# Kernel tuning notes

Measured on AMD Instinct MI355X. Metric: run time of the kernel, lower is better.

The kernel has to match this reference:

```python
import jax, jax.numpy as jnp
import numpy as np

STATE_DIM = 32
ACTION_DIM = 8
LATENT_DIM = 64
HIDDEN = 128
X_DIM = ACTION_DIM + 1  # t channel + actions
B = 4096
L = 128
N_SUB = 2  # fixed RK4 substeps per knot interval


def natural_cubic_coeffs(x):
    """Natural cubic spline on unit-spaced knots 0..L-1 (matches torchcde's
    implicit arange grid). x: [B, L, C]. Returns per-interval coeffs b, c, d
    ([B, L-1, C]) s.t. X(i+u) = x_i + b u + c u^2 + d u^3."""
    Bb, Ln, C = x.shape
    n = Ln - 2
    # tridiagonal system for interior second derivatives (natural BC: m0=mL-1=0)
    M = 4.0 * jnp.eye(n, dtype=x.dtype) + jnp.eye(n, k=1, dtype=x.dtype) + jnp.eye(n, k=-1, dtype=x.dtype)
    rhs = 6.0 * (x[:, 2:] - 2.0 * x[:, 1:-1] + x[:, :-2])  # [B, n, C]
    m_in = jnp.linalg.solve(M, rhs.transpose(1, 0, 2).reshape(n, -1))  # [n, B*C]
    m_in = m_in.reshape(n, Bb, C).transpose(1, 0, 2)
    zpad = jnp.zeros((Bb, 1, C), x.dtype)
    m = jnp.concatenate([zpad, m_in, zpad], axis=1)  # [B, L, C]
    b = (x[:, 1:] - x[:, :-1]) - (2.0 * m[:, :-1] + m[:, 1:]) / 6.0
    c = m[:, :-1] / 2.0
    d = (m[:, 1:] - m[:, :-1]) / 6.0
    return b, c, d


def setup_inputs() -> dict:
    key = jax.random.key(0)
    ks = jax.random.split(key, 8)
    s = jax.random.normal(ks[0], (B, L, STATE_DIM), dtype=jnp.float32)
    a = jax.random.normal(ks[1], (B, L, ACTION_DIM), dtype=jnp.float32)
    t = jnp.broadcast_to(jnp.arange(L, dtype=jnp.float32), (B, L)) + jnp.zeros((B, L), jnp.float32)

    def lin(k, fi, fo, scale=1.0):
        return (jax.random.normal(k, (fi, fo), dtype=jnp.float32) * (scale / np.sqrt(fi))).astype(jnp.float32)

    enc_W = lin(ks[2], STATE_DIM + ACTION_DIM + 1, LATENT_DIM)
    enc_b = jnp.zeros((LATENT_DIM,), jnp.float32)
    f_W1 = lin(ks[3], LATENT_DIM, HIDDEN, 0.5)
    f_b1 = jnp.zeros((HIDDEN,), jnp.float32)
    f_W2 = lin(ks[4], HIDDEN, LATENT_DIM * X_DIM, 0.1)  # small scale keeps the CDE stable over 127 time units
    f_b2 = jnp.zeros((LATENT_DIM * X_DIM,), jnp.float32)
    dec_W = lin(ks[5], LATENT_DIM, STATE_DIM)
    dec_b = jnp.zeros((STATE_DIM,), jnp.float32)
    return dict(s=s, a=a, t=t, enc_W=enc_W, enc_b=enc_b, f_W1=f_W1, f_b1=f_b1,
                f_W2=f_W2, f_b2=f_b2, dec_W=dec_W, dec_b=dec_b)


def reference(s, a, t, enc_W, enc_b, f_W1, f_b1, f_W2, f_b2, dec_W, dec_b):
    # control path X = [t, a] : [B, L, X_DIM]
    x = jnp.concatenate([t[..., None], a], axis=-1)
    cb, cc, cd = natural_cubic_coeffs(x)  # each [B, L-1, X_DIM]

    z0 = jnp.concatenate([s[:, 0], a[:, 0], t[:, 0:1]], axis=-1) @ enc_W + enc_b  # [B, latent]

    def vf(z):  # f(z): [B, latent] -> [B, latent, X_DIM]
        h = jax.nn.relu(z @ f_W1 + f_b1)
        return (h @ f_W2 + f_b2).reshape(-1, LATENT_DIM, X_DIM)

    hstep = 1.0 / N_SUB

    def interval(z, coef):
        bi, ci, di = coef  # [B, X_DIM] each, current interval spline coeffs

        def dzdu(z, u):
            dX = bi + 2.0 * ci * u + 3.0 * di * (u * u)  # dX/dt on this interval
            return jnp.einsum('blx,bx->bl', vf(z), dX)

        for k in range(N_SUB):  # small fixed unroll, not a data-dim loop
            u = k * hstep
            k1 = dzdu(z, u)
            k2 = dzdu(z + 0.5 * hstep * k1, u + 0.5 * hstep)
            k3 = dzdu(z + 0.5 * hstep * k2, u + 0.5 * hstep)
            k4 = dzdu(z + hstep * k3, u + hstep)
            z = z + (hstep / 6.0) * (k1 + 2.0 * k2 + 2.0 * k3 + k4)
        return z, z

    coefs = (cb.transpose(1, 0, 2), cc.transpose(1, 0, 2), cd.transpose(1, 0, 2))  # [L-1, B, X_DIM]
    _, zs = jax.lax.scan(interval, z0, coefs)  # zs: [L-1, B, latent]
    z = jnp.concatenate([z0[None], zs], axis=0).transpose(1, 0, 2)  # [B, L, latent]
    return z @ dec_W + dec_b  # [B, L, state_dim]
```

## Files before the change

### kernel.cpp

```cpp
#include <hip/hip_runtime.h>

#define Bsz 4096
#define Lsz 128
#define NI  127
#define SD  32
#define AD  8
#define LAT 64
#define HID 128
#define BT  16
#define THR 512

typedef float f32x2 __attribute__((ext_vector_type(2)));
typedef float f32x4 __attribute__((ext_vector_type(4)));

__global__ __launch_bounds__(256) void repack_w2(const float* __restrict__ W2,
                                                 float* __restrict__ W2p8,
                                                 float* __restrict__ W2c0){
  int idx = blockIdx.x*256 + threadIdx.x;
  if (idx < HID*LAT*8){
    int x = idx & 7; int jl = idx >> 3; int l = jl & 63; int j = jl >> 6;
    W2p8[idx] = W2[(j*LAT + l)*9 + x + 1];
  } else if (idx < HID*LAT*9){
    int jl = idx - HID*LAT*8;
    W2c0[jl] = W2[(size_t)jl*9];
  }
}

__global__ __launch_bounds__(256) void spline_kernel(const float* __restrict__ a,
                                                     float* __restrict__ m_ws){
  __shared__ float cp_s[126];
  if (threadIdx.x == 0){
    float c = 0.25f; cp_s[0] = c;
    for (int i=1;i<126;i++){ c = 1.0f/(4.0f - c); cp_s[i] = c; }
  }
  __syncthreads();
  int tid = blockIdx.x*256 + threadIdx.x;
  int b = tid >> 3, c8 = tid & 7;
  float dp[126];
  const float* ab = a + (size_t)b*Lsz*AD + c8;
  float x0 = ab[0];
  float x1 = ab[AD];
  for (int i=0;i<126;i++){
    float x2 = ab[(size_t)(i+2)*AD];
    float rhs = 6.0f*(x2 - 2.0f*x1 + x0);
    dp[i] = (i==0)? rhs*0.25f : (rhs - dp[i-1])*cp_s[i];
    x0 = x1; x1 = x2;
  }
  m_ws[tid] = 0.0f;
  m_ws[((size_t)127*Bsz)*8 + tid] = 0.0f;
  float mn = 0.0f;
  for (int k=125;k>=0;k--){
    mn = dp[k] - cp_s[k]*mn;
    m_ws[((size_t)(k+1)*Bsz)*8 + tid] = mn;
  }
}

#define DPP_XOR1(v) __int_as_float(__builtin_amdgcn_mov_dpp(__float_as_int(v), 0xB1, 0xF, 0xF, true))
#define DPP_XOR2(v) __int_as_float(__builtin_amdgcn_mov_dpp(__float_as_int(v), 0x4E, 0xF, 0xF, true))
#define SWZ_XOR4(v) __int_as_float(__builtin_amdgcn_ds_swizzle(__float_as_int(v), 0x101F))

#define PK_MUL_BCLO(d, w, x) asm("v_pk_mul_f32 %0, %1, %2 op_sel:[0,0] op_sel_hi:[0,1]" : "=v"(d) : "v"(w), "v"(x))
#define PK_MUL_BCHI(d, w, x) asm("v_pk_mul_f32 %0, %1, %2 op_sel:[1,0] op_sel_hi:[1,1]" : "=v"(d) : "v"(w), "v"(x))
#define PK_FMA_BCLO(acc, w, x) asm("v_pk_fma_f32 %0, %1, %2, %0 op_sel:[0,0,0] op_sel_hi:[0,1,1]" : "+v"(acc) : "v"(w), "v"(x))
#define PK_FMA_BCHI(acc, w, x) asm("v_pk_fma_f32 %0, %1, %2, %0 op_sel:[1,0,0] op_sel_hi:[1,1,1]" : "+v"(acc) : "v"(w), "v"(x))
#define PK_FMA(acc, a, b)      asm("v_pk_fma_f32 %0, %1, %2, %0" : "+v"(acc) : "v"(a), "v"(b))
#define PK_ADD(d, a, b)        asm("v_pk_add_f32 %0, %1, %2" : "=v"(d) : "v"(a), "v"(b))

#define LO2(v4) __builtin_shufflevector(v4, v4, 0, 1)
#define HI2(v4) __builtin_shufflevector(v4, v4, 2, 3)

__attribute__((amdgpu_waves_per_eu(2,2)))
__global__ __launch_bounds__(THR) void cde_integrate(
    const float* __restrict__ s, const float* __restrict__ a, const float* __restrict__ t,
    const float* __restrict__ encW, const float* __restrict__ encb,
    const float* __restrict__ W1, const float* __restrict__ b1,
    const float* __restrict__ b2, const float* __restrict__ decW, const float* __restrict__ decb,
    const float* __restrict__ W2p8, const float* __restrict__ W2c0, const float* __restrict__ m_ws,
    float* __restrict__ out)
{
  __shared__ float W1t[HID][LAT+4];
  __shared__ float hp[8][292];
  __shared__ float zp[8][132];
  __shared__ float dXp[5][8][20];
  __shared__ float dWs[LAT][SD];
  __shared__ float dbs[SD];

  const int tid = threadIdx.x;
  const int b0 = blockIdx.x * BT;
  const int ol = tid >> 3;
  const int jg = tid & 7;

  for (int i=tid;i<HID*LAT;i+=THR){ int j = i & (HID-1); int k = i >> 7; W1t[j][k] = W1[k*HID+j]; }
  for (int i=tid;i<LAT*SD;i+=THR)  ((float*)dWs)[i] = decW[i];
  if (tid < SD) dbs[tid] = decb[tid];

  f32x2 wpk[16][4]; f32x2 wc0pk[8];
  {
    #pragma unroll
    for (int jj=0;jj<16;jj++){
      const f32x2* p2 = (const f32x2*)&W2p8[((size_t)(jg*16+jj)*LAT + ol)*8];
      wpk[jj][0]=p2[0]; wpk[jj][1]=p2[1]; wpk[jj][2]=p2[2]; wpk[jj][3]=p2[3];
    }
    #pragma unroll
    for (int q=0;q<8;q++){
      wc0pk[q].x = W2c0[(jg*16+2*q)*LAT + ol];
      wc0pk[q].y = W2c0[(jg*16+2*q+1)*LAT + ol];
    }
    #pragma unroll
    for (int jj=0;jj<16;jj++){
      asm volatile("" : "+v"(wpk[jj][0]), "+v"(wpk[jj][1]), "+v"(wpk[jj][2]), "+v"(wpk[jj][3]));
    }
  }
  f32x2 b2p[4]; f32x2 b2c0v; f32x2 b1pair; f32x2 one11; one11.x = 1.f; one11.y = 1.f;
  {
    const float* bp = b2 + ol*9;
    b2c0v.x = bp[0]; b2c0v.y = 0.f;
    b2p[0].x = bp[1]; b2p[0].y = bp[2];
    b2p[1].x = bp[3]; b2p[1].y = bp[4];
    b2p[2].x = bp[5]; b2p[2].y = bp[6];
    b2p[3].x = bp[7]; b2p[3].y = bp[8];
    b1pair.x = b1[2*ol]; b1pair.y = b1[2*ol+1];
  }

  {
    const int bb8 = tid >> 6;
    const int li = tid & 63;
    #pragma unroll
    for (int h=0; h<2; h++){
      const int b = bb8 + 8*h;
      const float* sb = s + (size_t)(b0+b)*Lsz*SD;
      const float* ab = a + (size_t)(b0+b)*Lsz*AD;
      const float tv = t[(size_t)(b0+b)*Lsz];
      float acc = encb[li];
      #pragma unroll
      for (int k=0;k<SD;k++) acc = fmaf(sb[k], encW[k*LAT+li], acc);
      #pragma unroll
      for (int k=0;k<AD;k++) acc = fmaf(ab[k], encW[(SD+k)*LAT+li], acc);
      acc = fmaf(tv, encW[(SD+AD)*LAT+li], acc);
      zp[b>>1][li*2 + (b&1)] = acc;
    }
  }
  __syncthreads();

  {
    const int bb = tid >> 5; const int o = tid & 31; const int c = bb & 1;
    const float* zrow = &zp[bb>>1][0];
    float acc = dbs[o];
    #pragma unroll 16
    for (int k=0;k<LAT;k++) acc = fmaf(zrow[2*k+c], dWs[k][o], acc);
    out[((size_t)(b0+bb)*Lsz + 0)*SD + o] = acc;
  }

  float zb0, zb1, ka0 = 0.f, ka1 = 0.f;
  { f32x2 zr = *(const f32x2*)&zp[jg][2*ol]; zb0 = zr.x; zb1 = zr.y; }

  #pragma unroll 1
  for (int iv=0; iv<NI; iv++){
    for (int idx=tid; idx<5*BT*8; idx+=THR){
      int ui = idx >> 7; int r = idx & 127; int bb = r >> 3; int x8 = r & 7;
      float u = 0.25f*(float)ui;
      int gb = b0+bb;
      float m0 = m_ws[((size_t)iv    *Bsz + gb)*8 + x8];
      float m1 = m_ws[((size_t)(iv+1)*Bsz + gb)*8 + x8];
      float xd = a[((size_t)gb*Lsz + iv+1)*AD + x8] - a[((size_t)gb*Lsz + iv)*AD + x8];
      float cb = xd - (2.f*m0 + m1)*(1.f/6.f);
      float cc = 0.5f*m0;
      float cd = (m1 - m0)*(1.f/6.f);
      dXp[ui][bb>>1][x8*2 + (bb&1)] = cb + (2.f*cc)*u + (3.f*cd)*(u*u);
    }

    #pragma unroll 1
    for (int st=0; st<8; st++){
      const int ui = (st+1)>>1;
      const int mode = st & 3;
      __syncthreads();

      {
        const int j0 = 2*ol;
        f32x2 acc0, acc1;
        PK_MUL_BCLO(acc0, b1pair, one11);
        PK_MUL_BCHI(acc1, b1pair, one11);
        const f32x4* zrow = (const f32x4*)&zp[jg][0];
        const f32x4* w0r = (const f32x4*)&W1t[j0][0];
        const f32x4* w1r = (const f32x4*)&W1t[j0+1][0];
        #pragma unroll
        for (int k16=0;k16<16;k16++){
          f32x4 zqA = zrow[2*k16], zqB = zrow[2*k16+1];
          f32x4 w0q = w0r[k16], w1q = w1r[k16];
          f32x2 w0l = LO2(w0q), w0h = HI2(w0q), w1l = LO2(w1q), w1h = HI2(w1q);
          f32x2 zA0 = LO2(zqA), zA1 = HI2(zqA), zB0 = LO2(zqB), zB1 = HI2(zqB);
          PK_FMA_BCLO(acc0, w0l, zA0); PK_FMA_BCHI(acc0, w0l, zA1);
          PK_FMA_BCLO(acc0, w0h, zB0); PK_FMA_BCHI(acc0, w0h, zB1);
          PK_FMA_BCLO(acc1, w1l, zA0); PK_FMA_BCHI(acc1, w1l, zA1);
          PK_FMA_BCLO(acc1, w1h, zB0); PK_FMA_BCHI(acc1, w1h, zB1);
        }
        f32x4 hv;
        hv.x = fmaxf(acc0.x, 0.f); hv.y = fmaxf(acc0.y, 0.f);
        hv.z = fmaxf(acc1.x, 0.f); hv.w = fmaxf(acc1.y, 0.f);
        *(f32x4*)&hp[jg][(ol>>3)*36 + (ol&7)*4] = hv;
      }
      __syncthreads();

      f32x2 dz[8];
      #pragma unroll
      for (int p=0;p<8;p++){
        const f32x4* dxr = (const f32x4*)&dXp[ui][p][0];
        f32x4 d0=dxr[0], d1=dxr[1], d2=dxr[2], d3=dxr[3];
        f32x2 dx2[8] = {LO2(d0),HI2(d0),LO2(d1),HI2(d1),LO2(d2),HI2(d2),LO2(d3),HI2(d3)};
        const f32x4* hr = (const f32x4*)&hp[p][jg*36];
        f32x2 acc; acc.x = 0.f; acc.y = 0.f;
        #pragma unroll
        for (int jj2=0;jj2<8;jj2++){
          f32x4 hq = hr[jj2];
          f32x2 hl = LO2(hq), hh = HI2(hq);
          {
            f32x2 wd;
            PK_MUL_BCLO(wd, wpk[2*jj2][0], dx2[0]); PK_FMA_BCHI(wd, wpk[2*jj2][0], dx2[1]);
            PK_FMA_BCLO(wd, wpk[2*jj2][1], dx2[2]); PK_FMA_BCHI(wd, wpk[2*jj2][1], dx2[3]);
            PK_FMA_BCLO(wd, wpk[2*jj2][2], dx2[4]); PK_FMA_BCHI(wd, wpk[2*jj2][2], dx2[5]);
            PK_FMA_BCLO(wd, wpk[2*jj2][3], dx2[6]); PK_FMA_BCHI(wd, wpk[2*jj2][3], dx2[7]);
            PK_FMA_BCLO(wd, wc0pk[jj2], one11);
            PK_FMA(acc, hl, wd);
          }
          {
            f32x2 wd;
            PK_MUL_BCLO(wd, wpk[2*jj2+1][0], dx2[0]); PK_FMA_BCHI(wd, wpk[2*jj2+1][0], dx2[1]);
            PK_FMA_BCLO(wd, wpk[2*jj2+1][1], dx2[2]); PK_FMA_BCHI(wd, wpk[2*jj2+1][1], dx2[3]);
            PK_FMA_BCLO(wd, wpk[2*jj2+1][2], dx2[4]); PK_FMA_BCHI(wd, wpk[2*jj2+1][2], dx2[5]);
            PK_FMA_BCLO(wd, wpk[2*jj2+1][3], dx2[6]); PK_FMA_BCHI(wd, wpk[2*jj2+1][3], dx2[7]);
            PK_FMA_BCHI(wd, wc0pk[jj2], one11);
            PK_FMA(acc, hh, wd);
          }
        }
        dz[p] = acc;
      }

      const bool g1 = jg & 1;
      f32x2 n4[4];
      #pragma unroll
      for (int i=0;i<4;i++){
        f32x2 lo = dz[2*i], hi = dz[2*i+1];
        f32x2 send = g1 ? lo : hi;
        f32x2 recv; recv.x = DPP_XOR1(send.x); recv.y = DPP_XOR1(send.y);
        f32x2 keep = g1 ? hi : lo;
        PK_ADD(n4[i], keep, recv);
      }
      const bool g2 = jg & 2;
      f32x2 n2[2];
      #pragma unroll
      for (int i=0;i<2;i++){
        f32x2 lo = n4[2*i], hi = n4[2*i+1];
        f32x2 send = g2 ? lo : hi;
        f32x2 recv; recv.x = DPP_XOR2(send.x); recv.y = DPP_XOR2(send.y);
        f32x2 keep = g2 ? hi : lo;
        PK_ADD(n2[i], keep, recv);
      }
      const bool g4 = jg & 4;
      f32x2 res;
      {
        f32x2 lo = n2[0], hi = n2[1];
        f32x2 send = g4 ? lo : hi;
        f32x2 recv; recv.x = SWZ_XOR4(send.x); recv.y = SWZ_XOR4(send.y);
        f32x2 keep = g4 ? hi : lo;
        PK_ADD(res, keep, recv);
      }

      f32x2 bias2;
      {
        const f32x4* dxb = (const f32x4*)&dXp[ui][jg][0];
        f32x4 e0=dxb[0], e1=dxb[1], e2=dxb[2], e3=dxb[3];
        PK_MUL_BCLO(bias2, b2c0v, one11);
        PK_FMA_BCLO(bias2, b2p[0], LO2(e0)); PK_FMA_BCHI(bias2, b2p[0], HI2(e0));
        PK_FMA_BCLO(bias2, b2p[1], LO2(e1)); PK_FMA_BCHI(bias2, b2p[1], HI2(e1));
        PK_FMA_BCLO(bias2, b2p[2], LO2(e2)); PK_FMA_BCHI(bias2, b2p[2], HI2(e2));
        PK_FMA_BCLO(bias2, b2p[3], LO2(e3)); PK_FMA_BCHI(bias2, b2p[3], HI2(e3));
      }
      f32x2 dzm2; PK_ADD(dzm2, res, bias2);
      const float dz0 = dzm2.x, dz1 = dzm2.y;

      float zn0, zn1;
      if (mode == 0){
        ka0 = dz0; ka1 = dz1;
        zn0 = fmaf(0.25f, dz0, zb0); zn1 = fmaf(0.25f, dz1, zb1);
      } else if (mode == 1){
        ka0 = fmaf(2.f, dz0, ka0); ka1 = fmaf(2.f, dz1, ka1);
        zn0 = fmaf(0.25f, dz0, zb0); zn1 = fmaf(0.25f, dz1, zb1);
      } else if (mode == 2){
        ka0 = fmaf(2.f, dz0, ka0); ka1 = fmaf(2.f, dz1, ka1);
        zn0 = fmaf(0.5f, dz0, zb0); zn1 = fmaf(0.5f, dz1, zb1);
      } else {
        ka0 += dz0; ka1 += dz1;
        zb0 = fmaf(0.5f/6.f, ka0, zb0); zb1 = fmaf(0.5f/6.f, ka1, zb1);
        zn0 = zb0; zn1 = zb1;
      }
      f32x2 zw; zw.x = zn0; zw.y = zn1;
      *(f32x2*)&zp[jg][2*ol] = zw;
    }

    __syncthreads();
    {
      const int bb = tid >> 5; const int o = tid & 31; const int c = bb & 1;
      const float* zrow = &zp[bb>>1][0];
      float acc = dbs[o];
      #pragma unroll 16
      for (int k=0;k<LAT;k++) acc = fmaf(zrow[2*k+c], dWs[k][o], acc);
      out[((size_t)(b0+bb)*Lsz + (iv+1))*SD + o] = acc;
    }
  }
}

extern "C" void kernel_launch(void* const* d_in, const int* in_sizes, int n_in,
                              void* d_out, int out_size, void* d_ws, size_t ws_size,
                              hipStream_t stream){
  const float* s    = (const float*)d_in[0];
  const float* a    = (const float*)d_in[1];
  const float* t    = (const float*)d_in[2];
  const float* encW = (const float*)d_in[3];
  const float* encb = (const float*)d_in[4];
  const float* W1   = (const float*)d_in[5];
  const float* b1   = (const float*)d_in[6];
  const float* W2   = (const float*)d_in[7];
  const float* b2   = (const float*)d_in[8];
  const float* decW = (const float*)d_in[9];
  const float* decb = (const float*)d_in[10];
  float* out = (float*)d_out;
  float* ws  = (float*)d_ws;
  float* W2p8 = ws;
  float* W2c0 = ws + HID*LAT*8;
  float* m_ws = ws + HID*LAT*9;

  hipLaunchKernelGGL(repack_w2, dim3((HID*LAT*9+255)/256), dim3(256), 0, stream, W2, W2p8, W2c0);
  hipLaunchKernelGGL(spline_kernel, dim3(Bsz*8/256), dim3(256), 0, stream, a, m_ws);
  hipLaunchKernelGGL(cde_integrate, dim3(Bsz/BT), dim3(THR), 0, stream,
                     s,a,t,encW,encb,W1,b1,b2,decW,decb,W2p8,W2c0,m_ws,out);
}
```

Measured before the change: 8.486 ms.

## Double threads per block and split hidden/W2 reductions across lane pairs

Raises the block to 1024 threads with 4 waves per EU and splits the work of each output lane across 16 threads instead of 8. The first layer halves its K loop and combines the halves with a swizzle, and the second layer holds half as many W2 weights per thread in registers, adding one more xor-8 reduction step. The b2 bias is moved into shared memory. The aim is to cut per-thread register pressure and serial work so more waves hide latency, at the cost of extra cross-lane shuffles, and in the first layer half the threads do redundant work and sit idle at the write.

```diff
diff --git a/kernel.cpp b/kernel.cpp
--- a/kernel.cpp
+++ b/kernel.cpp
@@ -8,7 +8,7 @@
 #define LAT 64
 #define HID 128
 #define BT  16
-#define THR 512
+#define THR 1024
 
 typedef float f32x2 __attribute__((ext_vector_type(2)));
 typedef float f32x4 __attribute__((ext_vector_type(4)));
@@ -58,18 +58,18 @@
 #define DPP_XOR1(v) __int_as_float(__builtin_amdgcn_mov_dpp(__float_as_int(v), 0xB1, 0xF, 0xF, true))
 #define DPP_XOR2(v) __int_as_float(__builtin_amdgcn_mov_dpp(__float_as_int(v), 0x4E, 0xF, 0xF, true))
 #define SWZ_XOR4(v) __int_as_float(__builtin_amdgcn_ds_swizzle(__float_as_int(v), 0x101F))
+#define SWZ_XOR8(v) __int_as_float(__builtin_amdgcn_ds_swizzle(__float_as_int(v), 0x201F))
 
 #define PK_MUL_BCLO(d, w, x) asm("v_pk_mul_f32 %0, %1, %2 op_sel:[0,0] op_sel_hi:[0,1]" : "=v"(d) : "v"(w), "v"(x))
 #define PK_MUL_BCHI(d, w, x) asm("v_pk_mul_f32 %0, %1, %2 op_sel:[1,0] op_sel_hi:[1,1]" : "=v"(d) : "v"(w), "v"(x))
 #define PK_FMA_BCLO(acc, w, x) asm("v_pk_fma_f32 %0, %1, %2, %0 op_sel:[0,0,0] op_sel_hi:[0,1,1]" : "+v"(acc) : "v"(w), "v"(x))
 #define PK_FMA_BCHI(acc, w, x) asm("v_pk_fma_f32 %0, %1, %2, %0 op_sel:[1,0,0] op_sel_hi:[1,1,1]" : "+v"(acc) : "v"(w), "v"(x))
 #define PK_FMA(acc, a, b)      asm("v_pk_fma_f32 %0, %1, %2, %0" : "+v"(acc) : "v"(a), "v"(b))
-#define PK_ADD(d, a, b)        asm("v_pk_add_f32 %0, %1, %2" : "=v"(d) : "v"(a), "v"(b))
 
 #define LO2(v4) __builtin_shufflevector(v4, v4, 0, 1)
 #define HI2(v4) __builtin_shufflevector(v4, v4, 2, 3)
 
-__attribute__((amdgpu_waves_per_eu(2,2)))
+__attribute__((amdgpu_waves_per_eu(4,4)))
 __global__ __launch_bounds__(THR) void cde_integrate(
     const float* __restrict__ s, const float* __restrict__ a, const float* __restrict__ t,
     const float* __restrict__ encW, const float* __restrict__ encb,
@@ -79,70 +79,60 @@
     float* __restrict__ out)
 {
   __shared__ float W1t[HID][LAT+4];
-  __shared__ float hp[8][292];
+  __shared__ float hp[8][324];
   __shared__ float zp[8][132];
   __shared__ float dXp[5][8][20];
+  __shared__ float b2s[LAT][12];
   __shared__ float dWs[LAT][SD];
   __shared__ float dbs[SD];
 
   const int tid = threadIdx.x;
   const int b0 = blockIdx.x * BT;
-  const int ol = tid >> 3;
-  const int jg = tid & 7;
+  const int ol = tid >> 4;
+  const int jg = tid & 15;
+  const int pown = jg & 7;
+  const int kh = (tid >> 3) & 1;
+  const int bp = tid & 7;
 
   for (int i=tid;i<HID*LAT;i+=THR){ int j = i & (HID-1); int k = i >> 7; W1t[j][k] = W1[k*HID+j]; }
   for (int i=tid;i<LAT*SD;i+=THR)  ((float*)dWs)[i] = decW[i];
+  for (int i=tid;i<LAT*12;i+=THR){ int l=i/12, x=i%12; b2s[l][x] = (x<9)? b2[l*9+x] : 0.f; }
   if (tid < SD) dbs[tid] = decb[tid];
 
-  f32x2 wpk[16][4]; f32x2 wc0pk[8];
+  f32x2 wpk[8][4]; f32x2 wc0[4];
   {
     #pragma unroll
-    for (int jj=0;jj<16;jj++){
-      const f32x2* p2 = (const f32x2*)&W2p8[((size_t)(jg*16+jj)*LAT + ol)*8];
-      wpk[jj][0]=p2[0]; wpk[jj][1]=p2[1]; wpk[jj][2]=p2[2]; wpk[jj][3]=p2[3];
+    for (int jj=0;jj<8;jj++){
+      const f32x4* p4 = (const f32x4*)&W2p8[((size_t)(jg*8+jj)*LAT + ol)*8];
+      f32x4 A = p4[0], B = p4[1];
+      wpk[jj][0]=LO2(A); wpk[jj][1]=HI2(A); wpk[jj][2]=LO2(B); wpk[jj][3]=HI2(B);
     }
     #pragma unroll
-    for (int q=0;q<8;q++){
-      wc0pk[q].x = W2c0[(jg*16+2*q)*LAT + ol];
-      wc0pk[q].y = W2c0[(jg*16+2*q+1)*LAT + ol];
-    }
+    for (int q=0;q<4;q++){
+      wc0[q].x = W2c0[(jg*8+2*q)*LAT + ol];
+      wc0[q].y = W2c0[(jg*8+2*q+1)*LAT + ol];
+    }
+  }
+  f32x2 b1pair; b1pair.x = b1[2*ol]; b1pair.y = b1[2*ol+1];
+  f32x2 one11; one11.x = 1.f; one11.y = 1.f;
+
+  {
+    const int b = tid >> 6;
+    const int li = tid & 63;
+    const float* sb = s + (size_t)(b0+b)*Lsz*SD;
+    const float* ab = a + (size_t)(b0+b)*Lsz*AD;
+    const float tv = t[(size_t)(b0+b)*Lsz];
+    float acc = encb[li];
     #pragma unroll
-    for (int jj=0;jj<16;jj++){
-      asm volatile("" : "+v"(wpk[jj][0]), "+v"(wpk[jj][1]), "+v"(wpk[jj][2]), "+v"(wpk[jj][3]));
-    }
-  }
-  f32x2 b2p[4]; f32x2 b2c0v; f32x2 b1pair; f32x2 one11; one11.x = 1.f; one11.y = 1.f;
-  {
-    const float* bp = b2 + ol*9;
-    b2c0v.x = bp[0]; b2c0v.y = 0.f;
-    b2p[0].x = bp[1]; b2p[0].y = bp[2];
-    b2p[1].x = bp[3]; b2p[1].y = bp[4];
-    b2p[2].x = bp[5]; b2p[2].y = bp[6];
-    b2p[3].x = bp[7]; b2p[3].y = bp[8];
-    b1pair.x = b1[2*ol]; b1pair.y = b1[2*ol+1];
-  }
-
-  {
-    const int bb8 = tid >> 6;
-    const int li = tid & 63;
+    for (int k=0;k<SD;k++) acc = fmaf(sb[k], encW[k*LAT+li], acc);
     #pragma unroll
-    for (int h=0; h<2; h++){
-      const int b = bb8 + 8*h;
-      const float* sb = s + (size_t)(b0+b)*Lsz*SD;
-      const float* ab = a + (size_t)(b0+b)*Lsz*AD;
-      const float tv = t[(size_t)(b0+b)*Lsz];
-      float acc = encb[li];
-      #pragma unroll
-      for (int k=0;k<SD;k++) acc = fmaf(sb[k], encW[k*LAT+li], acc);
-      #pragma unroll
-      for (int k=0;k<AD;k++) acc = fmaf(ab[k], encW[(SD+k)*LAT+li], acc);
-      acc = fmaf(tv, encW[(SD+AD)*LAT+li], acc);
-      zp[b>>1][li*2 + (b&1)] = acc;
-    }
+    for (int k=0;k<AD;k++) acc = fmaf(ab[k], encW[(SD+k)*LAT+li], acc);
+    acc = fmaf(tv, encW[(SD+AD)*LAT+li], acc);
+    zp[b>>1][li*2 + (b&1)] = acc;
   }
   __syncthreads();
 
-  {
+  if (tid < BT*SD){
     const int bb = tid >> 5; const int o = tid & 31; const int c = bb & 1;
     const float* zrow = &zp[bb>>1][0];
     float acc = dbs[o];
@@ -151,13 +141,13 @@
     out[((size_t)(b0+bb)*Lsz + 0)*SD + o] = acc;
   }
 
-  float zb0, zb1, ka0 = 0.f, ka1 = 0.f;
-  { f32x2 zr = *(const f32x2*)&zp[jg][2*ol]; zb0 = zr.x; zb1 = zr.y; }
+  f32x2 zb, ka;
+  { zb = *(const f32x2*)&zp[pown][2*ol]; ka.x = 0.f; ka.y = 0.f; }
 
   #pragma unroll 1
   for (int iv=0; iv<NI; iv++){
-    for (int idx=tid; idx<5*BT*8; idx+=THR){
-      int ui = idx >> 7; int r = idx & 127; int bb = r >> 3; int x8 = r & 7;
+    if (tid < 5*BT*8){
+      int ui = tid >> 7; int r = tid & 127; int bb = r >> 3; int x8 = r & 7;
       float u = 0.25f*(float)ui;
       int gb = b0+bb;
       float m0 = m_ws[((size_t)iv    *Bsz + gb)*8 + x8];
@@ -176,129 +166,135 @@
       __syncthreads();
 
       {
-        const int j0 = 2*ol;
         f32x2 acc0, acc1;
         PK_MUL_BCLO(acc0, b1pair, one11);
         PK_MUL_BCHI(acc1, b1pair, one11);
-        const f32x4* zrow = (const f32x4*)&zp[jg][0];
-        const f32x4* w0r = (const f32x4*)&W1t[j0][0];
-        const f32x4* w1r = (const f32x4*)&W1t[j0+1][0];
+        const f32x4* zr  = (const f32x4*)&zp[bp][kh*64];
+        const f32x4* w0r = (const f32x4*)&W1t[2*ol][kh*32];
+        const f32x4* w1r = (const f32x4*)&W1t[2*ol+1][kh*32];
         #pragma unroll
-        for (int k16=0;k16<16;k16++){
-          f32x4 zqA = zrow[2*k16], zqB = zrow[2*k16+1];
-          f32x4 w0q = w0r[k16], w1q = w1r[k16];
+        for (int c4=0;c4<8;c4++){
+          f32x4 w0q = w0r[c4], w1q = w1r[c4];
+          f32x4 zA = zr[2*c4], zB = zr[2*c4+1];
           f32x2 w0l = LO2(w0q), w0h = HI2(w0q), w1l = LO2(w1q), w1h = HI2(w1q);
-          f32x2 zA0 = LO2(zqA), zA1 = HI2(zqA), zB0 = LO2(zqB), zB1 = HI2(zqB);
-          PK_FMA_BCLO(acc0, w0l, zA0); PK_FMA_BCHI(acc0, w0l, zA1);
-          PK_FMA_BCLO(acc0, w0h, zB0); PK_FMA_BCHI(acc0, w0h, zB1);
-          PK_FMA_BCLO(acc1, w1l, zA0); PK_FMA_BCHI(acc1, w1l, zA1);
-          PK_FMA_BCLO(acc1, w1h, zB0); PK_FMA_BCHI(acc1, w1h, zB1);
+          f32x2 z0 = LO2(zA), z1 = HI2(zA), z2 = LO2(zB), z3 = HI2(zB);
+          PK_FMA_BCLO(acc0, w0l, z0); PK_FMA_BCHI(acc0, w0l, z1);
+          PK_FMA_BCLO(acc0, w0h, z2); PK_FMA_BCHI(acc0, w0h, z3);
+          PK_FMA_BCLO(acc1, w1l, z0); PK_FMA_BCHI(acc1, w1l, z1);
+          PK_FMA_BCLO(acc1, w1h, z2); PK_FMA_BCHI(acc1, w1h, z3);
         }
-        f32x4 hv;
-        hv.x = fmaxf(acc0.x, 0.f); hv.y = fmaxf(acc0.y, 0.f);
-        hv.z = fmaxf(acc1.x, 0.f); hv.w = fmaxf(acc1.y, 0.f);
-        *(f32x4*)&hp[jg][(ol>>3)*36 + (ol&7)*4] = hv;
+        acc0.x += SWZ_XOR8(acc0.x); acc0.y += SWZ_XOR8(acc0.y);
+        acc1.x += SWZ_XOR8(acc1.x); acc1.y += SWZ_XOR8(acc1.y);
+        if (kh == 0){
+          f32x4 hv;
+          hv.x = fmaxf(acc0.x,0.f); hv.y = fmaxf(acc0.y,0.f);
+          hv.z = fmaxf(acc1.x,0.f); hv.w = fmaxf(acc1.y,0.f);
+          *(f32x4*)&hp[bp][(ol>>2)*20 + (ol&3)*4] = hv;
+        }
       }
       __syncthreads();
 
-      f32x2 dz[8];
+      f32x2 haA, haB;
       #pragma unroll
-      for (int p=0;p<8;p++){
-        const f32x4* dxr = (const f32x4*)&dXp[ui][p][0];
-        f32x4 d0=dxr[0], d1=dxr[1], d2=dxr[2], d3=dxr[3];
-        f32x2 dx2[8] = {LO2(d0),HI2(d0),LO2(d1),HI2(d1),LO2(d2),HI2(d2),LO2(d3),HI2(d3)};
-        const f32x4* hr = (const f32x4*)&hp[p][jg*36];
-        f32x2 acc; acc.x = 0.f; acc.y = 0.f;
+      for (int half=0; half<2; half++){
+        f32x2 dzv[4];
         #pragma unroll
-        for (int jj2=0;jj2<8;jj2++){
-          f32x4 hq = hr[jj2];
-          f32x2 hl = LO2(hq), hh = HI2(hq);
-          {
-            f32x2 wd;
-            PK_MUL_BCLO(wd, wpk[2*jj2][0], dx2[0]); PK_FMA_BCHI(wd, wpk[2*jj2][0], dx2[1]);
-            PK_FMA_BCLO(wd, wpk[2*jj2][1], dx2[2]); PK_FMA_BCHI(wd, wpk[2*jj2][1], dx2[3]);
-            PK_FMA_BCLO(wd, wpk[2*jj2][2], dx2[4]); PK_FMA_BCHI(wd, wpk[2*jj2][2], dx2[5]);
-            PK_FMA_BCLO(wd, wpk[2*jj2][3], dx2[6]); PK_FMA_BCHI(wd, wpk[2*jj2][3], dx2[7]);
-            PK_FMA_BCLO(wd, wc0pk[jj2], one11);
-            PK_FMA(acc, hl, wd);
-          }
-          {
-            f32x2 wd;
-            PK_MUL_BCLO(wd, wpk[2*jj2+1][0], dx2[0]); PK_FMA_BCHI(wd, wpk[2*jj2+1][0], dx2[1]);
-            PK_FMA_BCLO(wd, wpk[2*jj2+1][1], dx2[2]); PK_FMA_BCHI(wd, wpk[2*jj2+1][1], dx2[3]);
-            PK_FMA_BCLO(wd, wpk[2*jj2+1][2], dx2[4]); PK_FMA_BCHI(wd, wpk[2*jj2+1][2], dx2[5]);
-            PK_FMA_BCLO(wd, wpk[2*jj2+1][3], dx2[6]); PK_FMA_BCHI(wd, wpk[2*jj2+1][3], dx2[7]);
-            PK_FMA_BCHI(wd, wc0pk[jj2], one11);
-            PK_FMA(acc, hh, wd);
+        for (int i=0;i<4;i++){ dzv[i].x = 0.f; dzv[i].y = 0.f; }
+        #pragma unroll
+        for (int pi=0; pi<4; pi++){
+          const int p = half*4 + pi;
+          const f32x4* dxr = (const f32x4*)&dXp[ui][p][0];
+          f32x4 d0=dxr[0], d1=dxr[1], d2=dxr[2], d3=dxr[3];
+          f32x2 dxp0=LO2(d0), dxp1=HI2(d0), dxp2=LO2(d1), dxp3=HI2(d1);
+          f32x2 dxp4=LO2(d2), dxp5=HI2(d2), dxp6=LO2(d3), dxp7=HI2(d3);
+          const f32x4* hr = (const f32x4*)&hp[p][jg*20];
+          #pragma unroll
+          for (int q=0;q<4;q++){
+            f32x4 hq = hr[q];
+            f32x2 hl = LO2(hq), hh = HI2(hq);
+            const int ja = 2*q, jb = 2*q+1;
+            {
+              f32x2 wd;
+              PK_MUL_BCLO(wd, wc0[q], one11);
+              PK_FMA_BCLO(wd, wpk[ja][0], dxp0); PK_FMA_BCHI(wd, wpk[ja][0], dxp1);
+              PK_FMA_BCLO(wd, wpk[ja][1], dxp2); PK_FMA_BCHI(wd, wpk[ja][1], dxp3);
+              PK_FMA_BCLO(wd, wpk[ja][2], dxp4); PK_FMA_BCHI(wd, wpk[ja][2], dxp5);
+              PK_FMA_BCLO(wd, wpk[ja][3], dxp6); PK_FMA_BCHI(wd, wpk[ja][3], dxp7);
+              PK_FMA(dzv[pi], hl, wd);
+            }
+            {
+              f32x2 wd;
+              PK_MUL_BCHI(wd, wc0[q], one11);
+              PK_FMA_BCLO(wd, wpk[jb][0], dxp0); PK_FMA_BCHI(wd, wpk[jb][0], dxp1);
+              PK_FMA_BCLO(wd, wpk[jb][1], dxp2); PK_FMA_BCHI(wd, wpk[jb][1], dxp3);
+              PK_FMA_BCLO(wd, wpk[jb][2], dxp4); PK_FMA_BCHI(wd, wpk[jb][2], dxp5);
+              PK_FMA_BCLO(wd, wpk[jb][3], dxp6); PK_FMA_BCHI(wd, wpk[jb][3], dxp7);
+              PK_FMA(dzv[pi], hh, wd);
+            }
           }
         }
-        dz[p] = acc;
-      }
-
-      const bool g1 = jg & 1;
-      f32x2 n4[4];
-      #pragma unroll
-      for (int i=0;i<4;i++){
-        f32x2 lo = dz[2*i], hi = dz[2*i+1];
-        f32x2 send = g1 ? lo : hi;
-        f32x2 recv; recv.x = DPP_XOR1(send.x); recv.y = DPP_XOR1(send.y);
-        f32x2 keep = g1 ? hi : lo;
-        PK_ADD(n4[i], keep, recv);
-      }
-      const bool g2 = jg & 2;
-      f32x2 n2[2];
-      #pragma unroll
-      for (int i=0;i<2;i++){
-        f32x2 lo = n4[2*i], hi = n4[2*i+1];
-        f32x2 send = g2 ? lo : hi;
+        const bool g1 = jg & 1;
+        f32x2 n2[2];
+        #pragma unroll
+        for (int i=0;i<2;i++){
+          f32x2 keep = g1 ? dzv[2*i+1] : dzv[2*i];
+          f32x2 send = g1 ? dzv[2*i]   : dzv[2*i+1];
+          f32x2 recv; recv.x = DPP_XOR1(send.x); recv.y = DPP_XOR1(send.y);
+          n2[i] = keep + recv;
+        }
+        const bool g2 = jg & 2;
+        f32x2 keep = g2 ? n2[1] : n2[0];
+        f32x2 send = g2 ? n2[0] : n2[1];
         f32x2 recv; recv.x = DPP_XOR2(send.x); recv.y = DPP_XOR2(send.y);
-        f32x2 keep = g2 ? hi : lo;
-        PK_ADD(n2[i], keep, recv);
-      }
-      const bool g4 = jg & 4;
-      f32x2 res;
+        f32x2 hres = keep + recv;
+        if (half==0) haA = hres; else haB = hres;
+      }
       {
-        f32x2 lo = n2[0], hi = n2[1];
-        f32x2 send = g4 ? lo : hi;
+        const bool g4 = jg & 4;
+        f32x2 keep = g4 ? haB : haA;
+        f32x2 send = g4 ? haA : haB;
         f32x2 recv; recv.x = SWZ_XOR4(send.x); recv.y = SWZ_XOR4(send.y);
-        f32x2 keep = g4 ? hi : lo;
-        PK_ADD(res, keep, recv);
-      }
+        haA = keep + recv;
+      }
+      { f32x2 r8; r8.x = SWZ_XOR8(haA.x); r8.y = SWZ_XOR8(haA.y); haA = haA + r8; }
 
       f32x2 bias2;
       {
-        const f32x4* dxb = (const f32x4*)&dXp[ui][jg][0];
-        f32x4 e0=dxb[0], e1=dxb[1], e2=dxb[2], e3=dxb[3];
-        PK_MUL_BCLO(bias2, b2c0v, one11);
-        PK_FMA_BCLO(bias2, b2p[0], LO2(e0)); PK_FMA_BCHI(bias2, b2p[0], HI2(e0));
-        PK_FMA_BCLO(bias2, b2p[1], LO2(e1)); PK_FMA_BCHI(bias2, b2p[1], HI2(e1));
-        PK_FMA_BCLO(bias2, b2p[2], LO2(e2)); PK_FMA_BCHI(bias2, b2p[2], HI2(e2));
-        PK_FMA_BCLO(bias2, b2p[3], LO2(e3)); PK_FMA_BCHI(bias2, b2p[3], HI2(e3));
-      }
-      f32x2 dzm2; PK_ADD(dzm2, res, bias2);
-      const float dz0 = dzm2.x, dz1 = dzm2.y;
-
-      float zn0, zn1;
+        const f32x4* bq = (const f32x4*)&b2s[ol][0];
+        f32x4 q0 = bq[0], q1 = bq[1], q2 = bq[2];
+        const f32x4* dxr = (const f32x4*)&dXp[ui][pown][0];
+        f32x4 d0=dxr[0], d1=dxr[1], d2=dxr[2], d3=dxr[3];
+        f32x2 e0=LO2(d0), e1=HI2(d0), e2=LO2(d1), e3=HI2(d1);
+        f32x2 e4=LO2(d2), e5=HI2(d2), e6=LO2(d3), e7=HI2(d3);
+        f32x2 q0l = LO2(q0), q0h = HI2(q0), q1l = LO2(q1), q1h = HI2(q1), q2l = LO2(q2);
+        PK_MUL_BCLO(bias2, q0l, one11);
+        PK_FMA_BCHI(bias2, q0l, e0);
+        PK_FMA_BCLO(bias2, q0h, e1);
+        PK_FMA_BCHI(bias2, q0h, e2);
+        PK_FMA_BCLO(bias2, q1l, e3);
+        PK_FMA_BCHI(bias2, q1l, e4);
+        PK_FMA_BCLO(bias2, q1h, e5);
+        PK_FMA_BCHI(bias2, q1h, e6);
+        PK_FMA_BCLO(bias2, q2l, e7);
+      }
+      f32x2 dzm = haA + bias2;
+
+      f32x2 zn;
       if (mode == 0){
-        ka0 = dz0; ka1 = dz1;
-        zn0 = fmaf(0.25f, dz0, zb0); zn1 = fmaf(0.25f, dz1, zb1);
+        ka = dzm;                    zn = zb + 0.25f*dzm;
       } else if (mode == 1){
-        ka0 = fmaf(2.f, dz0, ka0); ka1 = fmaf(2.f, dz1, ka1);
-        zn0 = fmaf(0.25f, dz0, zb0); zn1 = fmaf(0.25f, dz1, zb1);
+        ka = ka + 2.f*dzm;           zn = zb + 0.25f*dzm;
       } else if (mode == 2){
-        ka0 = fmaf(2.f, dz0, ka0); ka1 = fmaf(2.f, dz1, ka1);
-        zn0 = fmaf(0.5f, dz0, zb0); zn1 = fmaf(0.5f, dz1, zb1);
+        ka = ka + 2.f*dzm;           zn = zb + 0.5f*dzm;
       } else {
-        ka0 += dz0; ka1 += dz1;
-        zb0 = fmaf(0.5f/6.f, ka0, zb0); zb1 = fmaf(0.5f/6.f, ka1, zb1);
-        zn0 = zb0; zn1 = zb1;
-      }
-      f32x2 zw; zw.x = zn0; zw.y = zn1;
-      *(f32x2*)&zp[jg][2*ol] = zw;
+        ka = ka + dzm;               zb = zb + (0.5f/6.f)*ka;  zn = zb;
+      }
+      if (jg < 8) *(f32x2*)&zp[pown][2*ol] = zn;
+      if (mode != 3){  }
     }
 
     __syncthreads();
-    {
+    if (tid < BT*SD){
       const int bb = tid >> 5; const int o = tid & 31; const int c = bb & 1;
       const float* zrow = &zp[bb>>1][0];
       float acc = dbs[o];
```

Result: slower. 9.226 ms (+8.7%).
